# Kernel optimization log

Hardware: AMD Instinct MI355X
Metric: run time of the kernel (lower is better)

Reference implementation:

```python
import jax, jax.numpy as jnp
import numpy as np

B, C, H, W = 64, 2048, 24, 8
NUM_IDS = 751


def setup_inputs() -> dict:
    key = jax.random.key(0)
    k1, k2, k3 = jax.random.split(key, 3)
    features_map = jax.random.normal(k1, (B, C, H, W), dtype=jnp.float32)
    classifier_weight = jax.random.normal(k2, (NUM_IDS, C), dtype=jnp.float32) * 0.02
    pids = jax.random.randint(k3, (B,), 0, NUM_IDS, dtype=jnp.int64)
    return {"features_map": features_map, "classifier_weight": classifier_weight, "pids": pids}


def reference(features_map, classifier_weight, pids):
    b, c, h, w = features_map.shape
    # gather one classifier weight row per sample: [B, C]
    wrows = classifier_weight[pids]
    # per-sample 1xC @ Cx(H*W) matmul -> heatmap [B, H, W]
    heat = jnp.einsum('bc,bchw->bhw', wrows, features_map)
    hflat = heat.reshape(b, h * w)
    mn = hflat.min(axis=-1, keepdims=True)
    mx = hflat.max(axis=-1, keepdims=True)
    # original: normalize only if max != 0
    hflat = jnp.where(mx != 0, (hflat - mn) / (mx - mn), hflat)
    heat = jax.lax.stop_gradient(hflat.reshape(b, h, w))  # heatmap is detached
    return features_map * heat[:, None, :, :]
```

## Files before the change

### kernel.cpp

```cpp
#include <hip/hip_runtime.h>

#define BB 64
#define CC 2048
#define HWN 192
#define HW4 48
#define NCHUNK 16
#define CCHUNK 128
#define CSLICE 32
#define NSLICE (CC / CSLICE)

__global__ void __launch_bounds__(192) heat_partial_kernel(
    const float* __restrict__ f,
    const float* __restrict__ w,
    const int* __restrict__ pids,
    float* __restrict__ partial)
{
    const int blk = blockIdx.x;
    const int b = blk >> 4;
    const int k = blk & (NCHUNK - 1);
    const int tid = threadIdx.x;
    const int hw4 = tid % HW4;
    const int cl  = tid / HW4;

    __shared__ float ws[CCHUNK];
    __shared__ __align__(16) float4 red[HWN];

    const int row = pids[b];
    if (tid < CCHUNK) ws[tid] = w[(size_t)row * CC + k * CCHUNK + tid];
    __syncthreads();

    const size_t base = ((size_t)b * CC + (size_t)k * CCHUNK) * HW4;
    const float4* fb4 = (const float4*)f + base;

    float4 acc = make_float4(0.f, 0.f, 0.f, 0.f);
#pragma unroll 8
    for (int c = cl; c < CCHUNK; c += 4) {
        float4 v = fb4[(size_t)c * HW4 + hw4];
        float wv = ws[c];
        acc.x = fmaf(wv, v.x, acc.x);
        acc.y = fmaf(wv, v.y, acc.y);
        acc.z = fmaf(wv, v.z, acc.z);
        acc.w = fmaf(wv, v.w, acc.w);
    }
    red[tid] = acc;
    __syncthreads();
    if (tid < HW4) {
        float4 a0 = red[tid], a1 = red[tid + 48], a2 = red[tid + 96], a3 = red[tid + 144];
        float4 s = make_float4(a0.x + a1.x + a2.x + a3.x,
                               a0.y + a1.y + a2.y + a3.y,
                               a0.z + a1.z + a2.z + a3.z,
                               a0.w + a1.w + a2.w + a3.w);
        ((float4*)partial)[(size_t)(b * NCHUNK + k) * HW4 + tid] = s;
    }
}

__global__ void __launch_bounds__(256) norm_scale_kernel(
    const float* __restrict__ f,
    const float* __restrict__ partial,
    float* __restrict__ out)
{
    const int blk = blockIdx.x;
    const int b  = blk / NSLICE;
    const int ck = blk % NSLICE;
    const int tid = threadIdx.x;

    __shared__ __align__(16) float vals[HWN];
    __shared__ __align__(16) float hl[HWN];
    __shared__ float s_mn, s_mx;

    float v = 0.f;
    if (tid < HWN) {
        const float* pb = partial + (size_t)b * NCHUNK * HWN + tid;
#pragma unroll
        for (int kk = 0; kk < NCHUNK; ++kk)
            v += pb[(size_t)kk * HWN];
        vals[tid] = v;
    }
    __syncthreads();

    if (tid < 64) {
        float m0 = vals[tid], m1 = vals[tid + 64], m2 = vals[tid + 128];
        float mn = fminf(m0, fminf(m1, m2));
        float mx = fmaxf(m0, fmaxf(m1, m2));
        for (int off = 32; off > 0; off >>= 1) {
            mn = fminf(mn, __shfl_down(mn, off));
            mx = fmaxf(mx, __shfl_down(mx, off));
        }
        if (tid == 0) { s_mn = mn; s_mx = mx; }
    }
    __syncthreads();

    if (tid < HWN) {
        const float mn = s_mn, mx = s_mx;
        hl[tid] = (mx != 0.f) ? (v - mn) / (mx - mn) : v;
    }
    __syncthreads();

    const size_t base = ((size_t)b * CC + (size_t)ck * CSLICE) * HW4;
    const float4* fb4 = (const float4*)f + base;
    float4* ob4 = (float4*)out + base;
    const float4* h4 = (const float4*)hl;

#pragma unroll
    for (int it = 0; it < (CSLICE * HW4) / 256; ++it) {
        const int idx = it * 256 + tid;
        const int hw4 = idx % HW4;
        const float4 hv = h4[hw4];
        float4 x = fb4[idx];
        x.x *= hv.x; x.y *= hv.y; x.z *= hv.z; x.w *= hv.w;
        ob4[idx] = x;
    }
}

extern "C" void kernel_launch(void* const* d_in, const int* in_sizes, int n_in,
                              void* d_out, int out_size, void* d_ws, size_t ws_size,
                              hipStream_t stream) {
    const float* features = (const float*)d_in[0];
    const float* weight   = (const float*)d_in[1];
    const int*   pids     = (const int*)d_in[2];
    float* out = (float*)d_out;
    float* partial = (float*)d_ws;

    heat_partial_kernel<<<BB * NCHUNK, HWN, 0, stream>>>(features, weight, pids, partial);
    norm_scale_kernel<<<BB * NSLICE, 256, 0, stream>>>(features, partial, out);
}
```

Before: 195.2 us.

## Fuse heatmap and scale kernels with inter-block flag sync and register-held features

Merges the partial-heatmap and normalize/scale kernels into one launch. Each block keeps its feature tile in registers, publishes its partial sum plus a release flag, and spins until all chunks of its sample are ready. It then reduces the heatmap, normalizes it and writes the scaled output straight from registers. This is meant to remove the second full read of the feature map and the extra launch. In exchange it relies on all blocks of a sample being co-resident to avoid deadlock, and the flags are never reset, so later calls may read stale partials.

```diff
diff --git a/kernel.cpp b/kernel.cpp
--- a/kernel.cpp
+++ b/kernel.cpp
@@ -4,19 +4,21 @@
 #define CC 2048
 #define HWN 192
 #define HW4 48
-#define NCHUNK 16
-#define CCHUNK 128
-#define CSLICE 32
-#define NSLICE (CC / CSLICE)
+#define CCHUNK 64
+#define NCHUNK (CC / CCHUNK)
+#define CITER (CCHUNK / 4)
+#define MAGIC 0x5CA1AB1Eu
 
-__global__ void __launch_bounds__(192) heat_partial_kernel(
+__global__ void __launch_bounds__(192, 3) fused_kernel(
     const float* __restrict__ f,
     const float* __restrict__ w,
     const int* __restrict__ pids,
-    float* __restrict__ partial)
+    float* __restrict__ out,
+    float* __restrict__ partial,
+    unsigned int* __restrict__ flags)
 {
     const int blk = blockIdx.x;
-    const int b = blk >> 4;
+    const int b = blk >> 5;
     const int k = blk & (NCHUNK - 1);
     const int tid = threadIdx.x;
     const int hw4 = tid % HW4;
@@ -24,6 +26,8 @@
 
     __shared__ float ws[CCHUNK];
     __shared__ __align__(16) float4 red[HWN];
+    __shared__ __align__(16) float hl[HWN];
+    __shared__ float s_mn, s_mx;
 
     const int row = pids[b];
     if (tid < CCHUNK) ws[tid] = w[(size_t)row * CC + k * CCHUNK + tid];
@@ -32,15 +36,19 @@
     const size_t base = ((size_t)b * CC + (size_t)k * CCHUNK) * HW4;
     const float4* fb4 = (const float4*)f + base;
 
+    float4 r[CITER];
+#pragma unroll
+    for (int i = 0; i < CITER; ++i)
+        r[i] = fb4[(size_t)(cl + 4 * i) * HW4 + hw4];
+
     float4 acc = make_float4(0.f, 0.f, 0.f, 0.f);
-#pragma unroll 8
-    for (int c = cl; c < CCHUNK; c += 4) {
-        float4 v = fb4[(size_t)c * HW4 + hw4];
-        float wv = ws[c];
-        acc.x = fmaf(wv, v.x, acc.x);
-        acc.y = fmaf(wv, v.y, acc.y);
-        acc.z = fmaf(wv, v.z, acc.z);
-        acc.w = fmaf(wv, v.w, acc.w);
+#pragma unroll
+    for (int i = 0; i < CITER; ++i) {
+        const float wv = ws[cl + 4 * i];
+        acc.x = fmaf(wv, r[i].x, acc.x);
+        acc.y = fmaf(wv, r[i].y, acc.y);
+        acc.z = fmaf(wv, r[i].z, acc.z);
+        acc.w = fmaf(wv, r[i].w, acc.w);
     }
     red[tid] = acc;
     __syncthreads();
@@ -52,34 +60,32 @@
                                a0.w + a1.w + a2.w + a3.w);
         ((float4*)partial)[(size_t)(b * NCHUNK + k) * HW4 + tid] = s;
     }
-}
+    __threadfence();
+    __syncthreads();
+    if (tid == 0)
+        __hip_atomic_store(&flags[b * NCHUNK + k], MAGIC,
+                           __ATOMIC_RELEASE, __HIP_MEMORY_SCOPE_AGENT);
 
-__global__ void __launch_bounds__(256) norm_scale_kernel(
-    const float* __restrict__ f,
-    const float* __restrict__ partial,
-    float* __restrict__ out)
-{
-    const int blk = blockIdx.x;
-    const int b  = blk / NSLICE;
-    const int ck = blk % NSLICE;
-    const int tid = threadIdx.x;
-
-    __shared__ __align__(16) float vals[HWN];
-    __shared__ __align__(16) float hl[HWN];
-    __shared__ float s_mn, s_mx;
+    if (tid < NCHUNK) {
+        while (__hip_atomic_load(&flags[b * NCHUNK + tid],
+                                 __ATOMIC_ACQUIRE, __HIP_MEMORY_SCOPE_AGENT) != MAGIC)
+            __builtin_amdgcn_s_sleep(2);
+    }
+    __syncthreads();
+    __threadfence();
 
     float v = 0.f;
-    if (tid < HWN) {
+    {
         const float* pb = partial + (size_t)b * NCHUNK * HWN + tid;
 #pragma unroll
         for (int kk = 0; kk < NCHUNK; ++kk)
             v += pb[(size_t)kk * HWN];
-        vals[tid] = v;
     }
+    float* scratch = (float*)red;
+    scratch[tid] = v;
     __syncthreads();
-
     if (tid < 64) {
-        float m0 = vals[tid], m1 = vals[tid + 64], m2 = vals[tid + 128];
+        float m0 = scratch[tid], m1 = scratch[tid + 64], m2 = scratch[tid + 128];
         float mn = fminf(m0, fminf(m1, m2));
         float mx = fmaxf(m0, fmaxf(m1, m2));
         for (int off = 32; off > 0; off >>= 1) {
@@ -89,26 +95,19 @@
         if (tid == 0) { s_mn = mn; s_mx = mx; }
     }
     __syncthreads();
-
-    if (tid < HWN) {
+    {
         const float mn = s_mn, mx = s_mx;
         hl[tid] = (mx != 0.f) ? (v - mn) / (mx - mn) : v;
     }
     __syncthreads();
 
-    const size_t base = ((size_t)b * CC + (size_t)ck * CSLICE) * HW4;
-    const float4* fb4 = (const float4*)f + base;
+    const float4 hv = ((const float4*)hl)[hw4];
     float4* ob4 = (float4*)out + base;
-    const float4* h4 = (const float4*)hl;
-
 #pragma unroll
-    for (int it = 0; it < (CSLICE * HW4) / 256; ++it) {
-        const int idx = it * 256 + tid;
-        const int hw4 = idx % HW4;
-        const float4 hv = h4[hw4];
-        float4 x = fb4[idx];
+    for (int i = 0; i < CITER; ++i) {
+        float4 x = r[i];
         x.x *= hv.x; x.y *= hv.y; x.z *= hv.z; x.w *= hv.w;
-        ob4[idx] = x;
+        ob4[(size_t)(cl + 4 * i) * HW4 + hw4] = x;
     }
 }
 
@@ -119,8 +118,10 @@
     const float* weight   = (const float*)d_in[1];
     const int*   pids     = (const int*)d_in[2];
     float* out = (float*)d_out;
+
     float* partial = (float*)d_ws;
+    unsigned int* flags = (unsigned int*)(partial + (size_t)BB * NCHUNK * HWN);
 
-    heat_partial_kernel<<<BB * NCHUNK, HWN, 0, stream>>>(features, weight, pids, partial);
-    norm_scale_kernel<<<BB * NSLICE, 256, 0, stream>>>(features, partial, out);
+    fused_kernel<<<BB * NCHUNK, HWN, 0, stream>>>(features, weight, pids, out,
+                                                  partial, flags);
 }
```

Measured after the change: 634.1 us. 3.25x slower.
